# Kernel optimization log

Measured on AMD Instinct MI355X. Metric: run time of the kernel, lower is better.

The kernel has to match this reference:

```python
import jax, jax.numpy as jnp
import numpy as np

N = 50000      # nodes
E = 800000     # edges (before self-loops)
IN = 128       # in_dim
OUT = 128      # out_dim
H = 4          # heads
C = OUT // H   # per-head channels
G = 64         # number of graphs in batch
NEG_SLOPE = 0.2
GN_EPS = 1e-5


def setup_inputs() -> dict:
    key = jax.random.key(0)
    ks = jax.random.split(key, 6)
    x = jax.random.normal(ks[0], (N, IN), dtype=jnp.float32)
    edge_index = jax.random.randint(ks[1], (2, E), 0, N, dtype=jnp.int32)
    batch = jnp.sort(jax.random.randint(ks[2], (N,), 0, G, dtype=jnp.int32))
    # glorot-ish init for GATv2 params
    s = float(np.sqrt(6.0 / (IN + H * C)))
    Wl = jax.random.uniform(ks[3], (IN, H * C), jnp.float32, -s, s)  # source (lin_l)
    Wr = jax.random.uniform(ks[4], (IN, H * C), jnp.float32, -s, s)  # target (lin_r)
    sa = float(np.sqrt(6.0 / (C + 1)))
    att = jax.random.uniform(ks[5], (H, C), jnp.float32, -sa, sa)
    bias_conv = jnp.zeros((H * C,), jnp.float32)
    gn_weight = jnp.ones((OUT,), jnp.float32)
    gn_bias = jnp.zeros((OUT,), jnp.float32)
    gn_mean_scale = jnp.ones((OUT,), jnp.float32)
    return {"x": x, "edge_index": edge_index, "batch": batch,
            "Wl": Wl, "Wr": Wr, "att": att, "bias_conv": bias_conv,
            "gn_weight": gn_weight, "gn_bias": gn_bias, "gn_mean_scale": gn_mean_scale}


def reference(x, edge_index, batch, Wl, Wr, att, bias_conv, gn_weight, gn_bias, gn_mean_scale):
    n = x.shape[0]
    # --- GATv2Conv (eval: dropout off), add_self_loops=True ---
    loop = jnp.arange(n, dtype=edge_index.dtype)
    src = jnp.concatenate([edge_index[0], loop])  # source j
    dst = jnp.concatenate([edge_index[1], loop])  # target i
    xl = (x @ Wl).reshape(n, H, C)  # source-side features
    xr = (x @ Wr).reshape(n, H, C)  # target-side features
    m = xl[src] + xr[dst]                               # [E', H, C]
    e = jax.nn.leaky_relu(m, NEG_SLOPE)
    logits = jnp.einsum('ehc,hc->eh', e, att)           # [E', H]
    # segment softmax over destination nodes
    amax = jax.ops.segment_max(logits, dst, num_segments=n)   # [N, H]
    ex = jnp.exp(logits - amax[dst])
    denom = jax.ops.segment_sum(ex, dst, num_segments=n)      # [N, H]
    alpha = ex / (denom[dst] + 1e-16)
    out = jax.ops.segment_sum(alpha[:, :, None] * xl[src], dst, num_segments=n)  # [N, H, C]
    out = out.reshape(n, H * C) + bias_conv
    # --- GraphNorm: (x - a*mean_g) / sqrt(var_g + eps) * w + b ---
    ones = jnp.ones((n, 1), out.dtype)
    cnt = jnp.maximum(jax.ops.segment_sum(ones, batch, num_segments=G), 1.0)  # [G, 1]
    mean = jax.ops.segment_sum(out, batch, num_segments=G) / cnt             # [G, OUT]
    out_c = out - mean[batch] * gn_mean_scale
    var = jax.ops.segment_sum(out_c * out_c, batch, num_segments=G) / cnt    # [G, OUT]
    y = out_c / jnp.sqrt(var[batch] + GN_EPS) * gn_weight + gn_bias
    # --- ELU ---
    return jax.nn.elu(y)
```

## Files before the change

### kernel.cpp

```cpp
#include <hip/hip_runtime.h>
#include <math.h>

#define HH 4
#define GG 64
#define CHUNK 64
#define BDST 16
#define BSH  4
#define SLOT 768
#define NPT  16
#define HWORDS 3328
constexpr float NEG_SLOPE = 0.2f;
constexpr float GN_EPS = 1e-5f;

typedef __attribute__((ext_vector_type(8))) short bf16x8;
typedef __attribute__((ext_vector_type(4))) float f32x4;

__device__ __forceinline__ unsigned short f2bf_rne(float f) {
  unsigned u = __float_as_uint(f);
  u += 0x7fffu + ((u >> 16) & 1u);
  return (unsigned short)(u >> 16);
}

__global__ __launch_bounds__(256) void wpack(
    const float* __restrict__ Wl, const float* __restrict__ Wr,
    unsigned short* __restrict__ Bfrag) {
  int tid = blockIdx.x * 256 + threadIdx.x;
  int f = tid >> 6, l = tid & 63;
  int m = f >> 5;
  int t = (f >> 2) & 7;
  int ks = f & 3;
  int col = t * 16 + (l & 15);
  int k0 = ks * 32 + (l >> 4) * 8;
  const float* W = m ? Wr : Wl;
  unsigned short* dst = Bfrag + ((size_t)f * 64 + l) * 8;
  #pragma unroll
  for (int j = 0; j < 8; ++j)
    dst[j] = f2bf_rne(W[(k0 + j) * 128 + col]);
}

__global__ __launch_bounds__(256) void prep_merged(
    const int* __restrict__ ei, int* __restrict__ gcur, int* __restrict__ ebuf,
    int E, int E2, int nbk, int SB,
    const float* __restrict__ x, const unsigned short* __restrict__ Bfrag,
    const float* __restrict__ att,
    unsigned short* __restrict__ xlb, unsigned short* __restrict__ xrb,
    float* __restrict__ dA, float* __restrict__ dB, int n) {
  __shared__ int hist[HWORDS];
  const int t = threadIdx.x;
  if ((int)blockIdx.x < SB) {
    for (int i = t; i < HWORDS; i += 256) hist[i] = 0;
    __syncthreads();
    unsigned wcache[NPT];
    const int base = blockIdx.x * (256 * NPT);
    #pragma unroll
    for (int i = 0; i < NPT; ++i) {
      int e = base + i * 256 + t;
      unsigned w = 0xFFFFFFFFu;
      if (e < E2) {
        int src, dst;
        if (e < E) { src = ei[e]; dst = ei[E + e]; }
        else       { src = e - E; dst = e - E; }
        w = ((unsigned)(dst >> BSH) << 20) | ((unsigned)(dst & (BDST - 1)) << 16)
            | (unsigned)src;
        atomicAdd(&hist[dst >> BSH], 1);
      }
      wcache[i] = w;
    }
    __syncthreads();
    for (int b = t; b < nbk; b += 256) {
      int c = hist[b];
      if (c) hist[b] = atomicAdd(&gcur[b], c);
    }
    __syncthreads();
    #pragma unroll
    for (int i = 0; i < NPT; ++i) {
      unsigned w = wcache[i];
      if (w == 0xFFFFFFFFu) continue;
      int b = w >> 20;
      int pos = atomicAdd(&hist[b], 1);
      if (pos < SLOT) ebuf[b * SLOT + pos] = (int)(w & 0xFFFFF);
    }
    return;
  }
  const int wave = ((blockIdx.x - SB) * 256 + t) >> 6;
  if (wave * 16 >= n) return;
  const int l = t & 63;
  const int arow = min(wave * 16 + (l & 15), n - 1);
  const float4* xrow = reinterpret_cast<const float4*>(x + (size_t)arow * 128);

  bf16x8 a[4];
  #pragma unroll
  for (int ks = 0; ks < 4; ++ks) {
    float4 lo = xrow[ks * 8 + (l >> 4) * 2];
    float4 hi = xrow[ks * 8 + (l >> 4) * 2 + 1];
    bf16x8 v;
    v[0] = (short)f2bf_rne(lo.x); v[1] = (short)f2bf_rne(lo.y);
    v[2] = (short)f2bf_rne(lo.z); v[3] = (short)f2bf_rne(lo.w);
    v[4] = (short)f2bf_rne(hi.x); v[5] = (short)f2bf_rne(hi.y);
    v[6] = (short)f2bf_rne(hi.z); v[7] = (short)f2bf_rne(hi.w);
    a[ks] = v;
  }

  const int r0 = wave * 16 + (l >> 4) * 4;
  const int cb = l & 15;
  float pd[4] = {0.f, 0.f, 0.f, 0.f};
  #pragma unroll
  for (int tt = 0; tt < 8; ++tt) {
    f32x4 acc = {0.f, 0.f, 0.f, 0.f};
    #pragma unroll
    for (int ks = 0; ks < 4; ++ks) {
      const bf16x8* bp = reinterpret_cast<const bf16x8*>(
          Bfrag + ((size_t)((0 * 8 + tt) * 4 + ks) * 64 + l) * 8);
      acc = __builtin_amdgcn_mfma_f32_16x16x32_bf16(a[ks], *bp, acc, 0, 0, 0);
    }
    float attv = att[tt * 16 + cb];
    #pragma unroll
    for (int j = 0; j < 4; ++j) {
      int r = r0 + j;
      unsigned short h = f2bf_rne(acc[j]);
      if (r < n) xlb[(size_t)r * 128 + tt * 16 + cb] = h;
      pd[j] = fmaf(__uint_as_float((unsigned)h << 16), attv, pd[j]);
    }
    if (tt & 1) {
      #pragma unroll
      for (int j = 0; j < 4; ++j) {
        float v = pd[j];
        #pragma unroll
        for (int mk = 1; mk < 16; mk <<= 1) v += __shfl_xor(v, mk);
        if (cb == 0 && r0 + j < n) dA[(size_t)(r0 + j) * 4 + (tt >> 1)] = v;
        pd[j] = 0.f;
      }
    }
  }
  #pragma unroll
  for (int tt = 0; tt < 8; ++tt) {
    f32x4 acc = {0.f, 0.f, 0.f, 0.f};
    #pragma unroll
    for (int ks = 0; ks < 4; ++ks) {
      const bf16x8* bp = reinterpret_cast<const bf16x8*>(
          Bfrag + ((size_t)((1 * 8 + tt) * 4 + ks) * 64 + l) * 8);
      acc = __builtin_amdgcn_mfma_f32_16x16x32_bf16(a[ks], *bp, acc, 0, 0, 0);
    }
    float attv = att[tt * 16 + cb];
    #pragma unroll
    for (int j = 0; j < 4; ++j) {
      int r = r0 + j;
      unsigned short h = f2bf_rne(acc[j]);
      if (r < n) xrb[(size_t)r * 128 + tt * 16 + cb] = h;
      pd[j] = fmaf(__uint_as_float((unsigned)h << 16), attv, pd[j]);
    }
    if (tt & 1) {
      #pragma unroll
      for (int j = 0; j < 4; ++j) {
        float v = pd[j];
        #pragma unroll
        for (int mk = 1; mk < 16; mk <<= 1) v += __shfl_xor(v, mk);
        if (cb == 0 && r0 + j < n) dB[(size_t)(r0 + j) * 4 + (tt >> 1)] = v;
        pd[j] = 0.f;
      }
    }
  }
}

__global__ __launch_bounds__(256) void fused_aggr(
    const int* __restrict__ gcur, const int* __restrict__ ebuf,
    const unsigned char* __restrict__ xb,
    const unsigned char* __restrict__ xrb,
    const float* __restrict__ dA, const float* __restrict__ dB,
    const float* __restrict__ att, float* __restrict__ out, int n) {
  __shared__ int eraw[SLOT];
  __shared__ int elist[SLOT + 16];
  __shared__ int ldeg[BDST];
  __shared__ int lrow[BDST + 1];
  __shared__ int lcur[BDST];
  const int b = blockIdx.x;
  const int t = threadIdx.x;
  const int cnt = min(gcur[b], SLOT);
  if (t < BDST) ldeg[t] = 0;
  __syncthreads();
  for (int i = t; i < cnt; i += 256) {
    int w = ebuf[b * SLOT + i];
    eraw[i] = w;
    atomicAdd(&ldeg[(w >> 16) & (BDST - 1)], 1);
  }
  __syncthreads();
  if (t < BDST) {
    int v = ldeg[t];
    int incl = v;
    #pragma unroll
    for (int d = 1; d < BDST; d <<= 1) {
      int u = __shfl_up(incl, d);
      if (t >= d) incl += u;
    }
    lrow[t] = incl - v;
    lcur[t] = incl - v;
    if (t == BDST - 1) lrow[BDST] = incl;
  }
  __syncthreads();
  for (int i = t; i < cnt; i += 256) {
    int w = eraw[i];
    int pos = atomicAdd(&lcur[(w >> 16) & (BDST - 1)], 1);
    elist[pos] = (w & 0xFFFF) << 8;
  }
  if (t < 16) elist[cnt + t] = 0;
  __syncthreads();

  const int wv = t >> 6, lane = t & 63;
  const int u = lane & 15, gi = lane >> 4;
  const int hh = u >> 2;
  const float4 atA = *reinterpret_cast<const float4*>(att + u * 8);
  const float4 atB = *reinterpret_cast<const float4*>(att + u * 8 + 4);

  #define LDE(st) (*reinterpret_cast<const uint4*>( \
      xb + (size_t)(unsigned)ep[4 * (st) + gi] + u * 16))
  #define LDA(st) (dA[((unsigned)ep[4 * (st) + gi] >> 8) * 4 + hh])
  #define STEP(V, da, ebase) { \
    float x0 = __uint_as_float((V).x << 16); \
    float x1 = __uint_as_float((V).x & 0xffff0000u); \
    float x2 = __uint_as_float((V).y << 16); \
    float x3 = __uint_as_float((V).y & 0xffff0000u); \
    float x4 = __uint_as_float((V).z << 16); \
    float x5 = __uint_as_float((V).z & 0xffff0000u); \
    float x6 = __uint_as_float((V).w << 16); \
    float x7 = __uint_as_float((V).w & 0xffff0000u); \
    float p = fabsf(x0 + xr0) * atA.x; \
    p = fmaf(fabsf(x1 + xr1), atA.y, p); \
    p = fmaf(fabsf(x2 + xr2), atA.z, p); \
    p = fmaf(fabsf(x3 + xr3), atA.w, p); \
    p = fmaf(fabsf(x4 + xr4), atB.x, p); \
    p = fmaf(fabsf(x5 + xr5), atB.y, p); \
    p = fmaf(fabsf(x6 + xr6), atB.z, p); \
    p = fmaf(fabsf(x7 + xr7), atB.w, p); \
    p += __shfl_xor(p, 1); \
    p += __shfl_xor(p, 2); \
    float lg = fmaf(0.4f, p, fmaf(0.6f, (da), eB)); \
    float w = ((ebase) + gi < deg) ? __expf(lg) : 0.f; \
    s += w; \
    a0 = fmaf(w, x0, a0); a1 = fmaf(w, x1, a1); \
    a2 = fmaf(w, x2, a2); a3 = fmaf(w, x3, a3); \
    a4 = fmaf(w, x4, a4); a5 = fmaf(w, x5, a5); \
    a6 = fmaf(w, x6, a6); a7 = fmaf(w, x7, a7); }

  for (int j = 0; j < 4; ++j) {
    const int ldst = wv * 4 + j;
    const int node = b * BDST + ldst;
    if (node >= n) break;
    const uint4 xv = *reinterpret_cast<const uint4*>(xrb + (size_t)node * 256 + u * 16);
    const float xr0 = __uint_as_float(xv.x << 16);
    const float xr1 = __uint_as_float(xv.x & 0xffff0000u);
    const float xr2 = __uint_as_float(xv.y << 16);
    const float xr3 = __uint_as_float(xv.y & 0xffff0000u);
    const float xr4 = __uint_as_float(xv.z << 16);
    const float xr5 = __uint_as_float(xv.z & 0xffff0000u);
    const float xr6 = __uint_as_float(xv.w << 16);
    const float xr7 = __uint_as_float(xv.w & 0xffff0000u);
    const float eB = 0.6f * dB[(size_t)node * 4 + hh];
    const int k0 = lrow[ldst];
    const int deg = lrow[ldst + 1] - k0;
    const int* ep = elist + k0;

    uint4 V0 = LDE(0), V1 = LDE(1), V2 = LDE(2);
    float d0 = LDA(0), d1 = LDA(1), d2 = LDA(2);
    float s = 0.f;
    float a0 = 0.f, a1 = 0.f, a2 = 0.f, a3 = 0.f;
    float a4 = 0.f, a5 = 0.f, a6 = 0.f, a7 = 0.f;
    const int S = (deg + 3) >> 2;
    for (int i = 0; i < S; ++i) {
      uint4 C = V0; float dc = d0;
      V0 = V1; V1 = V2; d0 = d1; d1 = d2;
      V2 = LDE(i + 3); d2 = LDA(i + 3);
      STEP(C, dc, 4 * i)
    }
    s  += __shfl_xor(s, 16);  s  += __shfl_xor(s, 32);
    a0 += __shfl_xor(a0, 16); a0 += __shfl_xor(a0, 32);
    a1 += __shfl_xor(a1, 16); a1 += __shfl_xor(a1, 32);
    a2 += __shfl_xor(a2, 16); a2 += __shfl_xor(a2, 32);
    a3 += __shfl_xor(a3, 16); a3 += __shfl_xor(a3, 32);
    a4 += __shfl_xor(a4, 16); a4 += __shfl_xor(a4, 32);
    a5 += __shfl_xor(a5, 16); a5 += __shfl_xor(a5, 32);
    a6 += __shfl_xor(a6, 16); a6 += __shfl_xor(a6, 32);
    a7 += __shfl_xor(a7, 16); a7 += __shfl_xor(a7, 32);
    float inv = 1.f / (s + 1e-16f);
    if (gi == 0) {
      float* op = out + (size_t)node * 128 + u * 8;
      *reinterpret_cast<float4*>(op) =
          make_float4(a0 * inv, a1 * inv, a2 * inv, a3 * inv);
      *reinterpret_cast<float4*>(op + 4) =
          make_float4(a4 * inv, a5 * inv, a6 * inv, a7 * inv);
    }
  }
  #undef STEP
  #undef LDA
  #undef LDE
}

__global__ __launch_bounds__(128) void gn_stats(
    const float* __restrict__ out, const float* __restrict__ bias,
    const int* __restrict__ batch, float* __restrict__ gsum,
    float* __restrict__ gsumsq, int* __restrict__ gcnt, int n) {
  const int c = threadIdx.x;
  const int n0 = blockIdx.x * CHUNK;
  const int n1 = min(n0 + CHUNK, n);
  const float bc = bias[c];
  float bsum = 0.f, bsq = 0.f;
  int cnt = 0;
  int curg = batch[n0];
  for (int nid = n0; nid < n1; ++nid) {
    int g = batch[nid];
    if (g != curg) {
      atomicAdd(&gsum[curg * 128 + c], bsum);
      atomicAdd(&gsumsq[curg * 128 + c], bsq);
      if (c == 0) atomicAdd(&gcnt[curg], cnt);
      bsum = 0.f; bsq = 0.f; cnt = 0; curg = g;
    }
    float v = out[(size_t)nid * 128 + c] + bc;
    bsum += v; bsq += v * v; ++cnt;
  }
  atomicAdd(&gsum[curg * 128 + c], bsum);
  atomicAdd(&gsumsq[curg * 128 + c], bsq);
  if (c == 0) atomicAdd(&gcnt[curg], cnt);
}

__global__ __launch_bounds__(128) void gn_prep(
    const float* __restrict__ gsum, const float* __restrict__ gsumsq,
    const int* __restrict__ gcnt, const float* __restrict__ bias,
    const float* __restrict__ msc, const float* __restrict__ w,
    const float* __restrict__ b, float* __restrict__ K, float* __restrict__ S) {
  int g = blockIdx.x, c = threadIdx.x;
  float cnt = (float)max(gcnt[g], 1);
  float mean = gsum[g * 128 + c] / cnt;
  float a = msc[c];
  float var = gsumsq[g * 128 + c] / cnt - mean * mean * (2.f * a - a * a);
  float k = rsqrtf(var + GN_EPS) * w[c];
  K[g * 128 + c] = k;
  S[g * 128 + c] = (bias[c] - mean * a) * k + b[c];
}

__global__ __launch_bounds__(256) void gn_norm(
    float* __restrict__ out, const int* __restrict__ batch,
    const float* __restrict__ K, const float* __restrict__ S, int n) {
  int i = blockIdx.x * 256 + threadIdx.x;
  if (i >= n * 32) return;
  int nid = i >> 5, c4 = (i & 31) * 4;
  int g = batch[nid];
  const float4 k4 = *reinterpret_cast<const float4*>(K + g * 128 + c4);
  const float4 s4 = *reinterpret_cast<const float4*>(S + g * 128 + c4);
  float* op = out + (size_t)nid * 128 + c4;
  float4 v = *reinterpret_cast<const float4*>(op);
  v.x = fmaf(v.x, k4.x, s4.x); v.x = (v.x > 0.f) ? v.x : (__expf(v.x) - 1.f);
  v.y = fmaf(v.y, k4.y, s4.y); v.y = (v.y > 0.f) ? v.y : (__expf(v.y) - 1.f);
  v.z = fmaf(v.z, k4.z, s4.z); v.z = (v.z > 0.f) ? v.z : (__expf(v.z) - 1.f);
  v.w = fmaf(v.w, k4.w, s4.w); v.w = (v.w > 0.f) ? v.w : (__expf(v.w) - 1.f);
  *reinterpret_cast<float4*>(op) = v;
}

extern "C" void kernel_launch(void* const* d_in, const int* in_sizes, int n_in,
                              void* d_out, int out_size, void* d_ws, size_t ws_size,
                              hipStream_t stream) {
  const float* x    = (const float*)d_in[0];
  const int*   ei   = (const int*)d_in[1];
  const int*   batch= (const int*)d_in[2];
  const float* Wl   = (const float*)d_in[3];
  const float* Wr   = (const float*)d_in[4];
  const float* att  = (const float*)d_in[5];
  const float* bias = (const float*)d_in[6];
  const float* gw   = (const float*)d_in[7];
  const float* gb   = (const float*)d_in[8];
  const float* gms  = (const float*)d_in[9];
  float* out = (float*)d_out;

  const int n  = in_sizes[0] / 128;
  const int E  = in_sizes[1] / 2;
  const int E2 = E + n;
  const int NBK = (n + BDST - 1) / BDST;
  const int SB = (E2 + 256 * NPT - 1) / (256 * NPT);
  const int GB = (((n + 15) / 16) * 64 + 255) / 256;

  char* ws = (char*)d_ws;
  size_t off = 0;
  int*   gcur    = (int*)(ws + off); off += (size_t)((NBK + 63) & ~63) * 4;
  int*   gcnt    = (int*)(ws + off); off += GG * 4;
  float* gsum    = (float*)(ws + off); off += GG * 128 * 4;
  float* gsumsq  = (float*)(ws + off); off += GG * 128 * 4;
  size_t zero_bytes = off;
  int*   ebuf    = (int*)(ws + off); off += (size_t)NBK * SLOT * 4;
  unsigned short* xlb = (unsigned short*)(ws + off); off += (size_t)n * 128 * 2;
  unsigned short* xrb = (unsigned short*)(ws + off); off += (size_t)n * 128 * 2;
  float* dA      = (float*)(ws + off); off += (size_t)((n + 63) & ~63) * 4 * 4;
  float* dB      = (float*)(ws + off); off += (size_t)((n + 63) & ~63) * 4 * 4;
  unsigned short* Bfrag = (unsigned short*)(ws + off); off += 64 * 64 * 8 * 2;
  float* gK      = (float*)(ws + off); off += GG * 128 * 4;
  float* gS      = (float*)(ws + off); off += GG * 128 * 4;

  hipMemsetAsync(ws, 0, zero_bytes, stream);

  wpack<<<16, 256, 0, stream>>>(Wl, Wr, (unsigned short*)Bfrag);

  prep_merged<<<SB + GB, 256, 0, stream>>>(ei, gcur, ebuf, E, E2, NBK, SB,
                                           x, Bfrag, att, xlb, xrb, dA, dB, n);

  fused_aggr<<<NBK, 256, 0, stream>>>(gcur, ebuf, (const unsigned char*)xlb,
                                      (const unsigned char*)xrb, dA, dB,
                                      att, out, n);

  gn_stats<<<(n + CHUNK - 1) / CHUNK, 128, 0, stream>>>(out, bias, batch, gsum, gsumsq, gcnt, n);
  gn_prep<<<GG, 128, 0, stream>>>(gsum, gsumsq, gcnt, bias, gms, gw, gb, gK, gS);

  gn_norm<<<(n * 32 + 255) / 256, 256, 0, stream>>>(out, batch, gK, gS, n);
}
```

Before: 116.1 us.

## Merge two dst buckets per aggregation block, deepen prefetch, fold gn_prep into gn_norm

Each fused_aggr block now handles two 16-node destination buckets (32 nodes, 8 per wave), halving the grid and amortising the per-block edge sort. The software prefetch pipeline for edge features goes from 3 to 4 stages and skips loads past the end. The gn_prep kernel is removed and its per-group mean/variance arithmetic is recomputed inside gn_norm, saving one launch at the cost of redundant per-element math. The larger shared-memory footprint and longer per-block serial loop may reduce occupancy and load balance.

```diff
diff --git a/kernel.cpp b/kernel.cpp
--- a/kernel.cpp
+++ b/kernel.cpp
@@ -167,42 +167,46 @@
     const unsigned char* __restrict__ xb,
     const unsigned char* __restrict__ xrb,
     const float* __restrict__ dA, const float* __restrict__ dB,
-    const float* __restrict__ att, float* __restrict__ out, int n) {
-  __shared__ int eraw[SLOT];
-  __shared__ int elist[SLOT + 16];
-  __shared__ int ldeg[BDST];
-  __shared__ int lrow[BDST + 1];
-  __shared__ int lcur[BDST];
-  const int b = blockIdx.x;
+    const float* __restrict__ att, float* __restrict__ out, int n, int nbk) {
+  __shared__ int eraw[2 * SLOT];
+  __shared__ int elist[2 * SLOT + 32];
+  __shared__ int ldeg[32];
+  __shared__ int lrow[33];
+  __shared__ int lcur[32];
+  const int b0 = blockIdx.x * 2, b1 = b0 + 1;
   const int t = threadIdx.x;
-  const int cnt = min(gcur[b], SLOT);
-  if (t < BDST) ldeg[t] = 0;
+  const int cnt0 = min(gcur[b0], SLOT);
+  const int cnt1 = (b1 < nbk) ? min(gcur[b1], SLOT) : 0;
+  const int cnt = cnt0 + cnt1;
+  if (t < 32) ldeg[t] = 0;
   __syncthreads();
   for (int i = t; i < cnt; i += 256) {
-    int w = ebuf[b * SLOT + i];
-    eraw[i] = w;
-    atomicAdd(&ldeg[(w >> 16) & (BDST - 1)], 1);
+    bool sec = i >= cnt0;
+    int w = sec ? ebuf[b1 * SLOT + i - cnt0] : ebuf[b0 * SLOT + i];
+    int ld = ((w >> 16) & 15) | (sec ? 16 : 0);
+    eraw[i] = (w & 0xFFFF) | (ld << 16);
+    atomicAdd(&ldeg[ld], 1);
   }
   __syncthreads();
-  if (t < BDST) {
+  if (t < 32) {
     int v = ldeg[t];
     int incl = v;
     #pragma unroll
-    for (int d = 1; d < BDST; d <<= 1) {
-      int u = __shfl_up(incl, d);
-      if (t >= d) incl += u;
+    for (int d = 1; d < 32; d <<= 1) {
+      int uu = __shfl_up(incl, d);
+      if (t >= d) incl += uu;
     }
     lrow[t] = incl - v;
     lcur[t] = incl - v;
-    if (t == BDST - 1) lrow[BDST] = incl;
+    if (t == 31) lrow[32] = incl;
   }
   __syncthreads();
   for (int i = t; i < cnt; i += 256) {
     int w = eraw[i];
-    int pos = atomicAdd(&lcur[(w >> 16) & (BDST - 1)], 1);
+    int pos = atomicAdd(&lcur[(w >> 16) & 31], 1);
     elist[pos] = (w & 0xFFFF) << 8;
   }
-  if (t < 16) elist[cnt + t] = 0;
+  if (t < 32) elist[cnt + t] = 0;
   __syncthreads();
 
   const int wv = t >> 6, lane = t & 63;
@@ -241,9 +245,9 @@
     a4 = fmaf(w, x4, a4); a5 = fmaf(w, x5, a5); \
     a6 = fmaf(w, x6, a6); a7 = fmaf(w, x7, a7); }
 
-  for (int j = 0; j < 4; ++j) {
-    const int ldst = wv * 4 + j;
-    const int node = b * BDST + ldst;
+  for (int j = 0; j < 8; ++j) {
+    const int ldst = wv * 8 + j;
+    const int node = blockIdx.x * 32 + ldst;
     if (node >= n) break;
     const uint4 xv = *reinterpret_cast<const uint4*>(xrb + (size_t)node * 256 + u * 16);
     const float xr0 = __uint_as_float(xv.x << 16);
@@ -259,16 +263,17 @@
     const int deg = lrow[ldst + 1] - k0;
     const int* ep = elist + k0;
 
-    uint4 V0 = LDE(0), V1 = LDE(1), V2 = LDE(2);
-    float d0 = LDA(0), d1 = LDA(1), d2 = LDA(2);
+    uint4 V0 = LDE(0), V1 = LDE(1), V2 = LDE(2), V3 = LDE(3);
+    float d0 = LDA(0), d1 = LDA(1), d2 = LDA(2), d3 = LDA(3);
     float s = 0.f;
     float a0 = 0.f, a1 = 0.f, a2 = 0.f, a3 = 0.f;
     float a4 = 0.f, a5 = 0.f, a6 = 0.f, a7 = 0.f;
     const int S = (deg + 3) >> 2;
     for (int i = 0; i < S; ++i) {
       uint4 C = V0; float dc = d0;
-      V0 = V1; V1 = V2; d0 = d1; d1 = d2;
-      V2 = LDE(i + 3); d2 = LDA(i + 3);
+      V0 = V1; V1 = V2; V2 = V3;
+      d0 = d1; d1 = d2; d2 = d3;
+      if (i + 4 < S) { V3 = LDE(i + 4); d3 = LDA(i + 4); }
       STEP(C, dc, 4 * i)
     }
     s  += __shfl_xor(s, 16);  s  += __shfl_xor(s, 32);
@@ -321,36 +326,36 @@
   if (c == 0) atomicAdd(&gcnt[curg], cnt);
 }
 
-__global__ __launch_bounds__(128) void gn_prep(
+__global__ __launch_bounds__(256) void gn_norm(
+    float* __restrict__ out, const int* __restrict__ batch,
     const float* __restrict__ gsum, const float* __restrict__ gsumsq,
     const int* __restrict__ gcnt, const float* __restrict__ bias,
-    const float* __restrict__ msc, const float* __restrict__ w,
-    const float* __restrict__ b, float* __restrict__ K, float* __restrict__ S) {
-  int g = blockIdx.x, c = threadIdx.x;
-  float cnt = (float)max(gcnt[g], 1);
-  float mean = gsum[g * 128 + c] / cnt;
-  float a = msc[c];
-  float var = gsumsq[g * 128 + c] / cnt - mean * mean * (2.f * a - a * a);
-  float k = rsqrtf(var + GN_EPS) * w[c];
-  K[g * 128 + c] = k;
-  S[g * 128 + c] = (bias[c] - mean * a) * k + b[c];
-}
-
-__global__ __launch_bounds__(256) void gn_norm(
-    float* __restrict__ out, const int* __restrict__ batch,
-    const float* __restrict__ K, const float* __restrict__ S, int n) {
+    const float* __restrict__ msc, const float* __restrict__ gw,
+    const float* __restrict__ gb, int n) {
   int i = blockIdx.x * 256 + threadIdx.x;
   if (i >= n * 32) return;
   int nid = i >> 5, c4 = (i & 31) * 4;
   int g = batch[nid];
-  const float4 k4 = *reinterpret_cast<const float4*>(K + g * 128 + c4);
-  const float4 s4 = *reinterpret_cast<const float4*>(S + g * 128 + c4);
+  float cinv = 1.f / (float)max(gcnt[g], 1);
+  const float4 s4 = *reinterpret_cast<const float4*>(gsum + g * 128 + c4);
+  const float4 q4 = *reinterpret_cast<const float4*>(gsumsq + g * 128 + c4);
+  const float4 a4 = *reinterpret_cast<const float4*>(msc + c4);
+  const float4 w4 = *reinterpret_cast<const float4*>(gw + c4);
+  const float4 b4 = *reinterpret_cast<const float4*>(gb + c4);
+  const float4 bi4 = *reinterpret_cast<const float4*>(bias + c4);
   float* op = out + (size_t)nid * 128 + c4;
   float4 v = *reinterpret_cast<const float4*>(op);
-  v.x = fmaf(v.x, k4.x, s4.x); v.x = (v.x > 0.f) ? v.x : (__expf(v.x) - 1.f);
-  v.y = fmaf(v.y, k4.y, s4.y); v.y = (v.y > 0.f) ? v.y : (__expf(v.y) - 1.f);
-  v.z = fmaf(v.z, k4.z, s4.z); v.z = (v.z > 0.f) ? v.z : (__expf(v.z) - 1.f);
-  v.w = fmaf(v.w, k4.w, s4.w); v.w = (v.w > 0.f) ? v.w : (__expf(v.w) - 1.f);
+  #define NORM1(vc, sc, qc, ac, wc, bc, bic) { \
+    float mean = (sc) * cinv; \
+    float var = (qc) * cinv - mean * mean * (2.f * (ac) - (ac) * (ac)); \
+    float k = rsqrtf(var + GN_EPS) * (wc); \
+    vc = ((vc) + (bic) - mean * (ac)) * k + (bc); \
+    vc = ((vc) > 0.f) ? (vc) : (__expf(vc) - 1.f); }
+  NORM1(v.x, s4.x, q4.x, a4.x, w4.x, b4.x, bi4.x)
+  NORM1(v.y, s4.y, q4.y, a4.y, w4.y, b4.y, bi4.y)
+  NORM1(v.z, s4.z, q4.z, a4.z, w4.z, b4.z, bi4.z)
+  NORM1(v.w, s4.w, q4.w, a4.w, w4.w, b4.w, bi4.w)
+  #undef NORM1
   *reinterpret_cast<float4*>(op) = v;
 }
 
@@ -389,8 +394,6 @@
   float* dA      = (float*)(ws + off); off += (size_t)((n + 63) & ~63) * 4 * 4;
   float* dB      = (float*)(ws + off); off += (size_t)((n + 63) & ~63) * 4 * 4;
   unsigned short* Bfrag = (unsigned short*)(ws + off); off += 64 * 64 * 8 * 2;
-  float* gK      = (float*)(ws + off); off += GG * 128 * 4;
-  float* gS      = (float*)(ws + off); off += GG * 128 * 4;
 
   hipMemsetAsync(ws, 0, zero_bytes, stream);
 
@@ -399,12 +402,13 @@
   prep_merged<<<SB + GB, 256, 0, stream>>>(ei, gcur, ebuf, E, E2, NBK, SB,
                                            x, Bfrag, att, xlb, xrb, dA, dB, n);
 
-  fused_aggr<<<NBK, 256, 0, stream>>>(gcur, ebuf, (const unsigned char*)xlb,
-                                      (const unsigned char*)xrb, dA, dB,
-                                      att, out, n);
+  fused_aggr<<<(NBK + 1) / 2, 256, 0, stream>>>(gcur, ebuf,
+                                                (const unsigned char*)xlb,
+                                                (const unsigned char*)xrb, dA, dB,
+                                                att, out, n, NBK);
 
   gn_stats<<<(n + CHUNK - 1) / CHUNK, 128, 0, stream>>>(out, bias, batch, gsum, gsumsq, gcnt, n);
-  gn_prep<<<GG, 128, 0, stream>>>(gsum, gsumsq, gcnt, bias, gms, gw, gb, gK, gS);
-
-  gn_norm<<<(n * 32 + 255) / 256, 256, 0, stream>>>(out, batch, gK, gS, n);
-}
+
+  gn_norm<<<(n * 32 + 255) / 256, 256, 0, stream>>>(out, batch, gsum, gsumsq, gcnt,
+                                                    bias, gms, gw, gb, n);
+}
```

After: 125.1 us. +7.8%, slower.
